# Kernel tuning notes

Measured on AMD Instinct MI355X. Metric: run time of the kernel, lower is better.

## Reference

```python
import jax, jax.numpy as jnp
import numpy as np

NUM_CLASSES = 97  # vocab size; SOS token id == NUM_CLASSES
D = 512   # in_planes (xDim)
S = 512   # sDim (GRU hidden)
A = 512   # attDim == emdDim
T = 25    # max_len_labels == encoder length L
B = 2048  # batch


def setup_inputs() -> dict:
    key = jax.random.key(0)
    ks = jax.random.split(key, 15)
    r = lambda k, shp: jax.random.normal(k, shp, jnp.float32) * 0.05
    return dict(
        x=jax.random.normal(ks[0], (B, T, D), jnp.float32),
        targets=jax.random.randint(ks[1], (2, B, T), 0, NUM_CLASSES),  # (fwd, reversed)
        Wx=r(ks[2], (2, D, A)), bx=r(ks[3], (2, A)),
        Ws=r(ks[4], (2, S, A)), bs=r(ks[5], (2, A)),
        wv=r(ks[6], (2, A)), wvb=r(ks[7], (2,)),
        emb=r(ks[8], (2, NUM_CLASSES + 1, A)),
        Wih=r(ks[9], (2, 3 * S, D + A)), bih=r(ks[10], (2, 3 * S)),
        Whh=r(ks[11], (2, 3 * S, S)), bhh=r(ks[12], (2, 3 * S)),
        Wfc=r(ks[13], (2, NUM_CLASSES, S)), bfc=r(ks[14], (2, NUM_CLASSES)),
    )


def _decode(x, targets, Wx, bx, Ws, bs, wv, wvb, emb, Wih, bih, Whh, bhh, Wfc, bfc):
    """One DecoderUnit unrolled over T steps (teacher forcing). x: [B,L,D]."""
    Bn = x.shape[0]
    # xEmbed is step-invariant -> hoist out of the recurrence
    xProj = jnp.einsum('bld,da->bla', x, Wx) + bx  # [B,L,A]
    y0 = jnp.full((Bn, 1), NUM_CLASSES, dtype=targets.dtype)  # SOS at step 0
    y_seq = jnp.concatenate([y0, targets[:, :-1]], axis=1)     # [B,T]

    def step(s, y_prev):
        # Bahdanau attention
        sProj = s @ Ws + bs                                  # [B,A]
        e = jnp.tanh(sProj[:, None, :] + xProj) @ wv + wvb   # [B,L]
        alpha = jax.nn.softmax(e, axis=1)
        ctx = jnp.einsum('bl,bld->bd', alpha, x)             # [B,D]
        # single-step GRU (PyTorch gate convention: r, z, n)
        gin = jnp.concatenate([emb[y_prev], ctx], axis=1)    # [B, A+D]
        gi = gin @ Wih.T + bih                               # [B,3S]
        gh = s @ Whh.T + bhh
        ir, iz, inn = jnp.split(gi, 3, axis=1)
        hr, hz, hn = jnp.split(gh, 3, axis=1)
        r = jax.nn.sigmoid(ir + hr)
        z = jax.nn.sigmoid(iz + hz)
        n = jnp.tanh(inn + r * hn)
        s_new = (1.0 - z) * n + z * s
        return s_new, s_new @ Wfc.T + bfc                    # logits [B,C]

    s0 = jnp.zeros((Bn, S), x.dtype)
    _, outs = jax.lax.scan(step, s0, jnp.swapaxes(y_seq, 0, 1))  # [T,B,C]
    return jnp.swapaxes(outs, 0, 1)  # [B,T,C]


def reference(x, targets, Wx, bx, Ws, bs, wv, wvb, emb, Wih, bih, Whh, bhh, Wfc, bfc):
    # vmap over the 2 decoders (forward / reverse); x shared
    f = jax.vmap(_decode, in_axes=(None, 0) + (0,) * 13)
    return f(x, targets, Wx, bx, Ws, bs, wv, wvb, emb, Wih, bih, Whh, bhh, Wfc, bfc)  # [2,B,T,C]
```

## Files before the change

### kernel.cpp

```cpp
#include <hip/hip_runtime.h>
#include <hip/hip_fp16.h>

#define B_ 2048
#define T_ 25
#define CL_ 97

typedef float f32x4 __attribute__((ext_vector_type(4)));
typedef _Float16 f16x8 __attribute__((ext_vector_type(8)));
typedef _Float16 f16x2 __attribute__((ext_vector_type(2)));

#define DI static __device__ __forceinline__

DI float fast_tanh(float x) { return 1.0f - 2.0f / (__expf(2.0f * x) + 1.0f); }
DI float fast_sigm(float x) { return 1.0f / (1.0f + __expf(-x)); }


__global__ void k_convx(const float* __restrict__ x, _Float16* __restrict__ xh, int n8) {
    int i = blockIdx.x * 256 + threadIdx.x;
    if (i >= n8) return;
    const f32x4 v0 = *(const f32x4*)(x + (long long)i * 8);
    const f32x4 v1 = *(const f32x4*)(x + (long long)i * 8 + 4);
    f16x8 o;
    o[0] = (_Float16)v0[0]; o[1] = (_Float16)v0[1]; o[2] = (_Float16)v0[2]; o[3] = (_Float16)v0[3];
    o[4] = (_Float16)v1[0]; o[5] = (_Float16)v1[1]; o[6] = (_Float16)v1[2]; o[7] = (_Float16)v1[3];
    *(f16x8*)(xh + (long long)i * 8) = o;
}

__global__ void k_pack_w1(const float* __restrict__ Ws, const float* __restrict__ Whh,
                          const float* __restrict__ Wfc, const float* __restrict__ bs,
                          const float* __restrict__ bhh, const float* __restrict__ bfc,
                          _Float16* __restrict__ w1, float* __restrict__ b1) {
    int idx = blockIdx.x * 256 + threadIdx.x;
    if (idx >= 2 * 2176 * 64) return;
    const int k8 = idx & 63;
    const int n  = (idx >> 6) % 2176;
    const int g  = (idx >> 6) / 2176;
    const int k0 = k8 * 8;
    f16x8 o;
    if (n < 512) {
        const float* p = Ws + (long long)g * 512 * 512 + (long long)k0 * 512 + n;
        #pragma unroll
        for (int i = 0; i < 8; ++i) o[i] = (_Float16)p[(long long)i * 512];
    } else if (n < 2048) {
        const float* p = Whh + (long long)g * 1536 * 512 + (long long)(n - 512) * 512 + k0;
        #pragma unroll
        for (int i = 0; i < 8; ++i) o[i] = (_Float16)p[i];
    } else if (n < 2048 + CL_) {
        const float* p = Wfc + (long long)g * CL_ * 512 + (long long)(n - 2048) * 512 + k0;
        #pragma unroll
        for (int i = 0; i < 8; ++i) o[i] = (_Float16)p[i];
    } else {
        #pragma unroll
        for (int i = 0; i < 8; ++i) o[i] = (_Float16)0.0f;
    }
    *(f16x8*)(w1 + ((long long)g * 2176 + n) * 512 + k0) = o;
    if (k8 == 0) {
        float bv = (n < 512) ? bs[g * 512 + n]
                 : (n < 2048) ? bhh[g * 1536 + (n - 512)]
                 : (n < 2048 + CL_) ? bfc[g * CL_ + (n - 2048)] : 0.0f;
        b1[g * 2176 + n] = bv;
    }
}

__global__ void k_pack_w2(const float* __restrict__ Wih, _Float16* __restrict__ w2) {
    int idx = blockIdx.x * 256 + threadIdx.x;
    if (idx >= 2 * 1536 * 64) return;
    const int k8 = idx & 63;
    const int n  = (idx >> 6) % 1536;
    const int g  = (idx >> 6) / 1536;
    const int k0 = k8 * 8;
    const float* p = Wih + (long long)g * 1536 * 1024 + (long long)n * 1024 + 512 + k0;
    f16x8 o;
    #pragma unroll
    for (int i = 0; i < 8; ++i) o[i] = (_Float16)p[i];
    *(f16x8*)(w2 + ((long long)g * 1536 + n) * 512 + k0) = o;
}

__global__ void k_pack_wx(const float* __restrict__ Wx, _Float16* __restrict__ wx) {
    int idx = blockIdx.x * 256 + threadIdx.x;
    if (idx >= 2 * 512 * 64) return;
    const int k8 = idx & 63;
    const int n  = (idx >> 6) & 511;
    const int g  = (idx >> 6) >> 9;
    const int k0 = k8 * 8;
    const float* p = Wx + (long long)g * 512 * 512 + (long long)k0 * 512 + n;
    f16x8 o;
    #pragma unroll
    for (int i = 0; i < 8; ++i) o[i] = (_Float16)p[(long long)i * 512];
    *(f16x8*)(wx + ((long long)g * 512 + n) * 512 + k0) = o;
}

__global__ __launch_bounds__(256) void k_emb(const float* __restrict__ emb,
                                             const float* __restrict__ Wih,
                                             const float* __restrict__ bih,
                                             float* __restrict__ eW) {
    const int y = blockIdx.x;
    const int g = blockIdx.y;
    __shared__ float er[512];
    const int tid = threadIdx.x;
    for (int i = tid; i < 512; i += 256) er[i] = emb[(long long)(g * 98 + y) * 512 + i];
    __syncthreads();
    for (int j = tid; j < 1536; j += 256) {
        const float* wr = Wih + (long long)g * 1536 * 1024 + (long long)j * 1024;
        float acc = bih[g * 1536 + j];
        #pragma unroll 8
        for (int a = 0; a < 512; ++a) acc += er[a] * wr[a];
        eW[(long long)(g * 98 + y) * 1536 + j] = acc;
    }
}

__global__ __launch_bounds__(256) void gemm_bt(
    const _Float16* __restrict__ A, long long aG,
    const _Float16* __restrict__ B, long long bG,
    float* __restrict__ Cf, _Float16* __restrict__ Ch,
    long long cG, int ldc,
    const float* __restrict__ bias, int biasG,
    int nblk_off, int n_split,
    float* __restrict__ lout, int lcols, int lldc)
{
    __shared__ _Float16 As[128][72];
    __shared__ _Float16 Bs[128][72];
    const int g  = blockIdx.z;
    const int m0 = blockIdx.y * 128;
    const int n0 = (blockIdx.x + nblk_off) * 128;
    const _Float16* Ag = A + (long long)g * aG + (long long)m0 * 512;
    const _Float16* Bg = B + (long long)g * bG + (long long)n0 * 512;
    const int tid  = threadIdx.x;
    const int lane = tid & 63, w = tid >> 6;
    const int wr = w >> 1, wc = w & 1;
    const int lr = lane & 15, kg = lane >> 4;
    const int arow = tid >> 3;
    const int acol = (tid & 7) * 8;

    f32x4 acc[4][4];
    #pragma unroll
    for (int m = 0; m < 4; ++m)
        #pragma unroll
        for (int n = 0; n < 4; ++n) acc[m][n] = (f32x4)0.0f;

    for (int kt = 0; kt < 8; ++kt) {
        const int k0 = kt * 64;
        f16x8 ra[4], rb[4];
        #pragma unroll
        for (int i = 0; i < 4; ++i) {
            ra[i] = *(const f16x8*)(Ag + (long long)(arow + i * 32) * 512 + k0 + acol);
            rb[i] = *(const f16x8*)(Bg + (long long)(arow + i * 32) * 512 + k0 + acol);
        }
        __syncthreads();
        #pragma unroll
        for (int i = 0; i < 4; ++i) {
            *(f16x8*)&As[arow + i * 32][acol] = ra[i];
            *(f16x8*)&Bs[arow + i * 32][acol] = rb[i];
        }
        __syncthreads();
        #pragma unroll
        for (int kk = 0; kk < 2; ++kk) {
            f16x8 af[4], bf[4];
            #pragma unroll
            for (int m = 0; m < 4; ++m) af[m] = *(const f16x8*)&As[wr * 64 + m * 16 + lr][kk * 32 + kg * 8];
            #pragma unroll
            for (int n = 0; n < 4; ++n) bf[n] = *(const f16x8*)&Bs[wc * 64 + n * 16 + lr][kk * 32 + kg * 8];
            #pragma unroll
            for (int m = 0; m < 4; ++m)
                #pragma unroll
                for (int n = 0; n < 4; ++n)
                    acc[m][n] = __builtin_amdgcn_mfma_f32_16x16x32_f16(af[m], bf[n], acc[m][n], 0, 0, 0);
        }
    }

    #pragma unroll
    for (int n = 0; n < 4; ++n) {
        const int col = n0 + wc * 64 + n * 16 + lr;
        const float bb = bias ? bias[g * biasG + col] : 0.0f;
        if (col < n_split) {
            #pragma unroll
            for (int m = 0; m < 4; ++m) {
                const int row = m0 + wr * 64 + m * 16 + kg * 4;
                #pragma unroll
                for (int i = 0; i < 4; ++i) {
                    const long long off = (long long)g * cG + (long long)(row + i) * ldc + col;
                    const float v = acc[m][n][i] + bb;
                    if (Ch) Ch[off] = (_Float16)v; else Cf[off] = v;
                }
            }
        } else if (lout != nullptr) {
            const int c = col - n_split;
            if (c < lcols) {
                #pragma unroll
                for (int m = 0; m < 4; ++m) {
                    const int row = m0 + wr * 64 + m * 16 + kg * 4;
                    #pragma unroll
                    for (int i = 0; i < 4; ++i)
                        lout[(long long)(g * B_ + row + i) * lldc + c] = acc[m][n][i] + bb;
                }
            }
        }
    }
}

__global__ __launch_bounds__(256) void k_att(
    const float* __restrict__ Y,
    const _Float16* __restrict__ xpj,
    const _Float16* __restrict__ xh,
    const float* __restrict__ wv,
    _Float16* __restrict__ ctxh)
{
    const int b = blockIdx.x, g = blockIdx.z;
    const int tid = threadIdx.x, lane = tid & 63, w = tid >> 6;
    __shared__ float eL[25];
    const float* sp  = Y + (long long)(g * B_ + b) * 2048;
    const float* wvg = wv + g * 512;
    const int a0 = lane * 8;
    const f32x4 sp0 = *(const f32x4*)(sp + a0);
    const f32x4 sp1 = *(const f32x4*)(sp + a0 + 4);
    const f32x4 wv0 = *(const f32x4*)(wvg + a0);
    const f32x4 wv1 = *(const f32x4*)(wvg + a0 + 4);
    const _Float16* xpb = xpj + (long long)(g * B_ + b) * 25 * 512;
    for (int l = w; l < 25; l += 4) {
        const f16x8 xv = *(const f16x8*)(xpb + l * 512 + a0);
        float part = 0.0f;
        #pragma unroll
        for (int i = 0; i < 4; ++i) {
            part += fast_tanh(sp0[i] + (float)xv[i])     * wv0[i];
            part += fast_tanh(sp1[i] + (float)xv[4 + i]) * wv1[i];
        }
        #pragma unroll
        for (int off = 32; off > 0; off >>= 1) part += __shfl_xor(part, off);
        if (lane == 0) eL[l] = part;
    }
    __syncthreads();
    float m = -1e30f;
    #pragma unroll
    for (int l = 0; l < 25; ++l) m = fmaxf(m, eL[l]);
    float al[25], ssum = 0.0f;
    #pragma unroll
    for (int l = 0; l < 25; ++l) { al[l] = __expf(eL[l] - m); ssum += al[l]; }
    const float inv = 1.0f / ssum;
    const _Float16* xb = xh + (long long)b * 25 * 512;
    const int d0 = tid * 2;
    float c0 = 0.0f, c1 = 0.0f;
    #pragma unroll
    for (int l = 0; l < 25; ++l) {
        const f16x2 xv = *(const f16x2*)(xb + l * 512 + d0);
        c0 += al[l] * (float)xv[0];
        c1 += al[l] * (float)xv[1];
    }
    f16x2 o; o[0] = (_Float16)(c0 * inv); o[1] = (_Float16)(c1 * inv);
    *(f16x2*)(ctxh + (long long)(g * B_ + b) * 512 + d0) = o;
}

__global__ void k_gate(const float* __restrict__ Y,
                       const float* __restrict__ Y2,
                       const float* __restrict__ eW,
                       const int* __restrict__ tgt,
                       float* __restrict__ s32, _Float16* __restrict__ sh, int t)
{
    const int idx = blockIdx.x * 256 + threadIdx.x;
    if (idx >= 2 * B_ * 512) return;
    const int j = idx & 511;
    const int b = (idx >> 9) & (B_ - 1);
    const int g = idx >> 20;
    const int y = (t == 0) ? CL_ : tgt[(g * B_ + b) * T_ + t - 1];
    const float* ew = eW + (long long)(g * 98 + y) * 1536;
    const float* y2 = Y2 + (long long)(g * B_ + b) * 1536;
    const float* yy = Y  + (long long)(g * B_ + b) * 2048;
    const float r  = fast_sigm(ew[j]        + y2[j]        + yy[512 + j]);
    const float z  = fast_sigm(ew[512 + j]  + y2[512 + j]  + yy[1024 + j]);
    const float nn = fast_tanh(ew[1024 + j] + y2[1024 + j] + r * yy[1536 + j]);
    const long long si = (long long)(g * B_ + b) * 512 + j;
    const float sn = (1.0f - z) * nn + z * s32[si];
    s32[si] = sn;
    sh[si]  = (_Float16)sn;
}

extern "C" void kernel_launch(void* const* d_in, const int* in_sizes, int n_in,
                              void* d_out, int out_size, void* d_ws, size_t ws_size,
                              hipStream_t stream)
{
    (void)in_sizes; (void)n_in; (void)out_size;
    const float* x   = (const float*)d_in[0];
    const int*   tgt = (const int*)d_in[1];
    const float* Wx  = (const float*)d_in[2];
    const float* bx  = (const float*)d_in[3];
    const float* Wsm = (const float*)d_in[4];
    const float* bs  = (const float*)d_in[5];
    const float* wv  = (const float*)d_in[6];
    const float* emb = (const float*)d_in[8];
    const float* Wih = (const float*)d_in[9];
    const float* bih = (const float*)d_in[10];
    const float* Whh = (const float*)d_in[11];
    const float* bhh = (const float*)d_in[12];
    const float* Wfc = (const float*)d_in[13];
    const float* bfc = (const float*)d_in[14];
    float* out = (float*)d_out;

    char* base = (char*)d_ws;
    size_t off = 0;
    auto alloc = [&](size_t bytes) -> void* {
        void* r = base + off;
        off = (off + bytes + 255) & ~(size_t)255;
        return r;
    };
    _Float16* xh  = (_Float16*)alloc((size_t)B_ * T_ * 512 * 2);
    _Float16* xpj = (_Float16*)alloc((size_t)2 * B_ * T_ * 512 * 2);
    _Float16* w1  = (_Float16*)alloc((size_t)2 * 2176 * 512 * 2);
    _Float16* w2  = (_Float16*)alloc((size_t)2 * 1536 * 512 * 2);
    _Float16* wx  = (_Float16*)alloc((size_t)2 * 512 * 512 * 2);
    float*    b1  = (float*)alloc((size_t)2 * 2176 * 4);
    float*    eW  = (float*)alloc((size_t)2 * 98 * 1536 * 4);
    float*    s32 = (float*)alloc((size_t)2 * B_ * 512 * 4);
    _Float16* sh  = (_Float16*)alloc((size_t)2 * B_ * 512 * 2);
    _Float16* ctx = (_Float16*)alloc((size_t)2 * B_ * 512 * 2);
    float*    Y   = (float*)alloc((size_t)2 * B_ * 2048 * 4);
    float*    Y2  = (float*)alloc((size_t)2 * B_ * 1536 * 4);
    if (off > ws_size) return;

    hipMemsetAsync(s32, 0, (size_t)2 * B_ * 512 * 4, stream);
    hipMemsetAsync(sh,  0, (size_t)2 * B_ * 512 * 2, stream);

    k_convx  <<<12800, 256, 0, stream>>>(x, xh, (B_ * T_ * 512) / 8);
    k_pack_w1<<<1088, 256, 0, stream>>>(Wsm, Whh, Wfc, bs, bhh, bfc, w1, b1);
    k_pack_w2<<<768, 256, 0, stream>>>(Wih, w2);
    k_pack_wx<<<256, 256, 0, stream>>>(Wx, wx);
    k_emb    <<<dim3(98, 2), 256, 0, stream>>>(emb, Wih, bih, eW);

    gemm_bt<<<dim3(4, 400, 2), 256, 0, stream>>>(
        xh, 0ll, wx, 512ll * 512, nullptr, xpj, (long long)B_ * T_ * 512, 512,
        bx, 512, 0, 1 << 30, nullptr, 0, 0);

    for (int t = 0; t < T_; ++t) {
        gemm_bt<<<dim3(t > 0 ? 17 : 16, 16, 2), 256, 0, stream>>>(
            sh, (long long)B_ * 512, w1, 2176ll * 512, Y, nullptr,
            (long long)B_ * 2048, 2048, b1, 2176, 0, 2048,
            t > 0 ? out + (long long)(t - 1) * CL_ : nullptr, CL_, T_ * CL_);
        k_att<<<dim3(B_, 1, 2), 256, 0, stream>>>(Y, xpj, xh, wv, ctx);
        gemm_bt<<<dim3(12, 16, 2), 256, 0, stream>>>(
            ctx, (long long)B_ * 512, w2, 1536ll * 512, Y2, nullptr,
            (long long)B_ * 1536, 1536, nullptr, 0, 0, 1 << 30, nullptr, 0, 0);
        k_gate<<<8192, 256, 0, stream>>>(Y, Y2, eW, tgt, s32, sh, t);
    }
    gemm_bt<<<dim3(1, 16, 2), 256, 0, stream>>>(
        sh, (long long)B_ * 512, w1, 2176ll * 512, Y, nullptr,
        (long long)B_ * 2048, 2048, b1, 2176, 16, 2048,
        out + 24ll * CL_, CL_, T_ * CL_);
}
```

Before: 2.859 ms.

## Use direct global-to-LDS loads in GEMM, fp16 intermediates, MFMA embedding projection

The GEMM now stages tiles with global_load_lds (direct global-to-shared copies) into unpadded shared tiles, where before data went through registers. The per-step intermediates Y and Y2 are stored as fp16 instead of fp32, which roughly halves their traffic in the attention and gate kernels. The gate kernel processes two elements per thread. The scalar embedding×Wih precompute is replaced by a packed fp16 MFMA GEMM. Risks include LDS bank conflicts from removing the padding and reduced precision in the gate pre-activations.

```diff
diff --git a/kernel.cpp b/kernel.cpp
--- a/kernel.cpp
+++ b/kernel.cpp
@@ -6,6 +6,7 @@
 #define CL_ 97
 
 typedef float f32x4 __attribute__((ext_vector_type(4)));
+typedef float f32x2 __attribute__((ext_vector_type(2)));
 typedef _Float16 f16x8 __attribute__((ext_vector_type(8)));
 typedef _Float16 f16x2 __attribute__((ext_vector_type(2)));
 
@@ -13,6 +14,11 @@
 
 DI float fast_tanh(float x) { return 1.0f - 2.0f / (__expf(2.0f * x) + 1.0f); }
 DI float fast_sigm(float x) { return 1.0f / (1.0f + __expf(-x)); }
+
+DI void gl16(const void* g, void* l) {
+    __builtin_amdgcn_global_load_lds((const __attribute__((address_space(1))) void*)g,
+                                     (__attribute__((address_space(3))) void*)l, 16, 0, 0);
+}
 
 
 __global__ void k_convx(const float* __restrict__ x, _Float16* __restrict__ xh, int n8) {
@@ -62,18 +68,20 @@
     }
 }
 
-__global__ void k_pack_w2(const float* __restrict__ Wih, _Float16* __restrict__ w2) {
+__global__ void k_pack_w2(const float* __restrict__ Wih, _Float16* __restrict__ w2,
+                          _Float16* __restrict__ w2e) {
     int idx = blockIdx.x * 256 + threadIdx.x;
     if (idx >= 2 * 1536 * 64) return;
     const int k8 = idx & 63;
     const int n  = (idx >> 6) % 1536;
     const int g  = (idx >> 6) / 1536;
     const int k0 = k8 * 8;
-    const float* p = Wih + (long long)g * 1536 * 1024 + (long long)n * 1024 + 512 + k0;
-    f16x8 o;
-    #pragma unroll
-    for (int i = 0; i < 8; ++i) o[i] = (_Float16)p[i];
-    *(f16x8*)(w2 + ((long long)g * 1536 + n) * 512 + k0) = o;
+    const float* p = Wih + (long long)g * 1536 * 1024 + (long long)n * 1024;
+    f16x8 o, oe;
+    #pragma unroll
+    for (int i = 0; i < 8; ++i) { o[i] = (_Float16)p[512 + k0 + i]; oe[i] = (_Float16)p[k0 + i]; }
+    *(f16x8*)(w2  + ((long long)g * 1536 + n) * 512 + k0) = o;
+    *(f16x8*)(w2e + ((long long)g * 1536 + n) * 512 + k0) = oe;
 }
 
 __global__ void k_pack_wx(const float* __restrict__ Wx, _Float16* __restrict__ wx) {
@@ -90,23 +98,22 @@
     *(f16x8*)(wx + ((long long)g * 512 + n) * 512 + k0) = o;
 }
 
-__global__ __launch_bounds__(256) void k_emb(const float* __restrict__ emb,
-                                             const float* __restrict__ Wih,
-                                             const float* __restrict__ bih,
-                                             float* __restrict__ eW) {
-    const int y = blockIdx.x;
-    const int g = blockIdx.y;
-    __shared__ float er[512];
-    const int tid = threadIdx.x;
-    for (int i = tid; i < 512; i += 256) er[i] = emb[(long long)(g * 98 + y) * 512 + i];
-    __syncthreads();
-    for (int j = tid; j < 1536; j += 256) {
-        const float* wr = Wih + (long long)g * 1536 * 1024 + (long long)j * 1024;
-        float acc = bih[g * 1536 + j];
-        #pragma unroll 8
-        for (int a = 0; a < 512; ++a) acc += er[a] * wr[a];
-        eW[(long long)(g * 98 + y) * 1536 + j] = acc;
-    }
+__global__ void k_pack_emb(const float* __restrict__ emb, _Float16* __restrict__ embh) {
+    int i = blockIdx.x * 256 + threadIdx.x;
+    if (i >= 2 * 128 * 64) return;
+    const int k8 = i & 63;
+    const int y  = (i >> 6) & 127;
+    const int g  = i >> 13;
+    f16x8 o;
+    if (y < 98) {
+        const float* p = emb + (long long)(g * 98 + y) * 512 + k8 * 8;
+        #pragma unroll
+        for (int j = 0; j < 8; ++j) o[j] = (_Float16)p[j];
+    } else {
+        #pragma unroll
+        for (int j = 0; j < 8; ++j) o[j] = (_Float16)0.0f;
+    }
+    *(f16x8*)(embh + (long long)(g * 128 + y) * 512 + k8 * 8) = o;
 }
 
 __global__ __launch_bounds__(256) void gemm_bt(
@@ -118,8 +125,8 @@
     int nblk_off, int n_split,
     float* __restrict__ lout, int lcols, int lldc)
 {
-    __shared__ _Float16 As[128][72];
-    __shared__ _Float16 Bs[128][72];
+    __shared__ _Float16 As[128 * 64];
+    __shared__ _Float16 Bs[128 * 64];
     const int g  = blockIdx.z;
     const int m0 = blockIdx.y * 128;
     const int n0 = (blockIdx.x + nblk_off) * 128;
@@ -129,8 +136,8 @@
     const int lane = tid & 63, w = tid >> 6;
     const int wr = w >> 1, wc = w & 1;
     const int lr = lane & 15, kg = lane >> 4;
-    const int arow = tid >> 3;
-    const int acol = (tid & 7) * 8;
+    const int srow = (lane >> 3);
+    const int scol = (lane & 7) * 8;
 
     f32x4 acc[4][4];
     #pragma unroll
@@ -140,26 +147,21 @@
 
     for (int kt = 0; kt < 8; ++kt) {
         const int k0 = kt * 64;
-        f16x8 ra[4], rb[4];
-        #pragma unroll
-        for (int i = 0; i < 4; ++i) {
-            ra[i] = *(const f16x8*)(Ag + (long long)(arow + i * 32) * 512 + k0 + acol);
-            rb[i] = *(const f16x8*)(Bg + (long long)(arow + i * 32) * 512 + k0 + acol);
-        }
         __syncthreads();
         #pragma unroll
-        for (int i = 0; i < 4; ++i) {
-            *(f16x8*)&As[arow + i * 32][acol] = ra[i];
-            *(f16x8*)&Bs[arow + i * 32][acol] = rb[i];
+        for (int cc = 0; cc < 4; ++cc) {
+            const int r = w * 32 + cc * 8;
+            gl16(Ag + (long long)(r + srow) * 512 + k0 + scol, &As[r * 64]);
+            gl16(Bg + (long long)(r + srow) * 512 + k0 + scol, &Bs[r * 64]);
         }
         __syncthreads();
         #pragma unroll
         for (int kk = 0; kk < 2; ++kk) {
             f16x8 af[4], bf[4];
             #pragma unroll
-            for (int m = 0; m < 4; ++m) af[m] = *(const f16x8*)&As[wr * 64 + m * 16 + lr][kk * 32 + kg * 8];
+            for (int m = 0; m < 4; ++m) af[m] = *(const f16x8*)&As[(wr * 64 + m * 16 + lr) * 64 + kk * 32 + kg * 8];
             #pragma unroll
-            for (int n = 0; n < 4; ++n) bf[n] = *(const f16x8*)&Bs[wc * 64 + n * 16 + lr][kk * 32 + kg * 8];
+            for (int n = 0; n < 4; ++n) bf[n] = *(const f16x8*)&Bs[(wc * 64 + n * 16 + lr) * 64 + kk * 32 + kg * 8];
             #pragma unroll
             for (int m = 0; m < 4; ++m)
                 #pragma unroll
@@ -199,7 +201,7 @@
 }
 
 __global__ __launch_bounds__(256) void k_att(
-    const float* __restrict__ Y,
+    const _Float16* __restrict__ Yh,
     const _Float16* __restrict__ xpj,
     const _Float16* __restrict__ xh,
     const float* __restrict__ wv,
@@ -208,11 +210,10 @@
     const int b = blockIdx.x, g = blockIdx.z;
     const int tid = threadIdx.x, lane = tid & 63, w = tid >> 6;
     __shared__ float eL[25];
-    const float* sp  = Y + (long long)(g * B_ + b) * 2048;
+    const _Float16* sp = Yh + (long long)(g * B_ + b) * 2048;
     const float* wvg = wv + g * 512;
     const int a0 = lane * 8;
-    const f32x4 sp0 = *(const f32x4*)(sp + a0);
-    const f32x4 sp1 = *(const f32x4*)(sp + a0 + 4);
+    const f16x8 spv = *(const f16x8*)(sp + a0);
     const f32x4 wv0 = *(const f32x4*)(wvg + a0);
     const f32x4 wv1 = *(const f32x4*)(wvg + a0 + 4);
     const _Float16* xpb = xpj + (long long)(g * B_ + b) * 25 * 512;
@@ -221,8 +222,8 @@
         float part = 0.0f;
         #pragma unroll
         for (int i = 0; i < 4; ++i) {
-            part += fast_tanh(sp0[i] + (float)xv[i])     * wv0[i];
-            part += fast_tanh(sp1[i] + (float)xv[4 + i]) * wv1[i];
+            part += fast_tanh((float)spv[i]     + (float)xv[i])     * wv0[i];
+            part += fast_tanh((float)spv[4 + i] + (float)xv[4 + i]) * wv1[i];
         }
         #pragma unroll
         for (int off = 32; off > 0; off >>= 1) part += __shfl_xor(part, off);
@@ -249,28 +250,44 @@
     *(f16x2*)(ctxh + (long long)(g * B_ + b) * 512 + d0) = o;
 }
 
-__global__ void k_gate(const float* __restrict__ Y,
-                       const float* __restrict__ Y2,
+__global__ void k_gate(const _Float16* __restrict__ Yh,
+                       const _Float16* __restrict__ Y2h,
                        const float* __restrict__ eW,
                        const int* __restrict__ tgt,
                        float* __restrict__ s32, _Float16* __restrict__ sh, int t)
 {
     const int idx = blockIdx.x * 256 + threadIdx.x;
-    if (idx >= 2 * B_ * 512) return;
-    const int j = idx & 511;
-    const int b = (idx >> 9) & (B_ - 1);
-    const int g = idx >> 20;
-    const int y = (t == 0) ? CL_ : tgt[(g * B_ + b) * T_ + t - 1];
-    const float* ew = eW + (long long)(g * 98 + y) * 1536;
-    const float* y2 = Y2 + (long long)(g * B_ + b) * 1536;
-    const float* yy = Y  + (long long)(g * B_ + b) * 2048;
-    const float r  = fast_sigm(ew[j]        + y2[j]        + yy[512 + j]);
-    const float z  = fast_sigm(ew[512 + j]  + y2[512 + j]  + yy[1024 + j]);
-    const float nn = fast_tanh(ew[1024 + j] + y2[1024 + j] + r * yy[1536 + j]);
-    const long long si = (long long)(g * B_ + b) * 512 + j;
-    const float sn = (1.0f - z) * nn + z * s32[si];
-    s32[si] = sn;
-    sh[si]  = (_Float16)sn;
+    if (idx >= 2 * B_ * 256) return;
+    const int jp = (idx & 255) * 2;
+    const int b  = (idx >> 8) & (B_ - 1);
+    const int g  = idx >> 19;
+    const int y  = (t == 0) ? CL_ : tgt[(g * B_ + b) * T_ + t - 1];
+    const float*    ew = eW  + (long long)(g * 128 + y) * 1536;
+    const _Float16* y2 = Y2h + (long long)(g * B_ + b) * 1536;
+    const _Float16* yy = Yh  + (long long)(g * B_ + b) * 2048;
+    const f32x2 ewr = *(const f32x2*)(ew + jp);
+    const f32x2 ewz = *(const f32x2*)(ew + 512 + jp);
+    const f32x2 ewn = *(const f32x2*)(ew + 1024 + jp);
+    const f16x2 y2r = *(const f16x2*)(y2 + jp);
+    const f16x2 y2z = *(const f16x2*)(y2 + 512 + jp);
+    const f16x2 y2n = *(const f16x2*)(y2 + 1024 + jp);
+    const f16x2 ghr = *(const f16x2*)(yy + 512 + jp);
+    const f16x2 ghz = *(const f16x2*)(yy + 1024 + jp);
+    const f16x2 ghn = *(const f16x2*)(yy + 1536 + jp);
+    const long long si = (long long)(g * B_ + b) * 512 + jp;
+    const f32x2 so = *(const f32x2*)(s32 + si);
+    f32x2 sn;
+    f16x2 snh;
+    #pragma unroll
+    for (int i = 0; i < 2; ++i) {
+        const float r  = fast_sigm(ewr[i] + (float)y2r[i] + (float)ghr[i]);
+        const float z  = fast_sigm(ewz[i] + (float)y2z[i] + (float)ghz[i]);
+        const float nn = fast_tanh(ewn[i] + (float)y2n[i] + r * (float)ghn[i]);
+        sn[i]  = (1.0f - z) * nn + z * so[i];
+        snh[i] = (_Float16)sn[i];
+    }
+    *(f32x2*)(s32 + si) = sn;
+    *(f16x2*)(sh + si) = snh;
 }
 
 extern "C" void kernel_launch(void* const* d_in, const int* in_sizes, int n_in,
@@ -301,28 +318,34 @@
         off = (off + bytes + 255) & ~(size_t)255;
         return r;
     };
-    _Float16* xh  = (_Float16*)alloc((size_t)B_ * T_ * 512 * 2);
-    _Float16* xpj = (_Float16*)alloc((size_t)2 * B_ * T_ * 512 * 2);
-    _Float16* w1  = (_Float16*)alloc((size_t)2 * 2176 * 512 * 2);
-    _Float16* w2  = (_Float16*)alloc((size_t)2 * 1536 * 512 * 2);
-    _Float16* wx  = (_Float16*)alloc((size_t)2 * 512 * 512 * 2);
-    float*    b1  = (float*)alloc((size_t)2 * 2176 * 4);
-    float*    eW  = (float*)alloc((size_t)2 * 98 * 1536 * 4);
-    float*    s32 = (float*)alloc((size_t)2 * B_ * 512 * 4);
-    _Float16* sh  = (_Float16*)alloc((size_t)2 * B_ * 512 * 2);
-    _Float16* ctx = (_Float16*)alloc((size_t)2 * B_ * 512 * 2);
-    float*    Y   = (float*)alloc((size_t)2 * B_ * 2048 * 4);
-    float*    Y2  = (float*)alloc((size_t)2 * B_ * 1536 * 4);
+    _Float16* xh   = (_Float16*)alloc((size_t)B_ * T_ * 512 * 2);
+    _Float16* xpj  = (_Float16*)alloc((size_t)2 * B_ * T_ * 512 * 2);
+    _Float16* w1   = (_Float16*)alloc((size_t)2 * 2176 * 512 * 2);
+    _Float16* w2   = (_Float16*)alloc((size_t)2 * 1536 * 512 * 2);
+    _Float16* w2e  = (_Float16*)alloc((size_t)2 * 1536 * 512 * 2);
+    _Float16* wx   = (_Float16*)alloc((size_t)2 * 512 * 512 * 2);
+    _Float16* embh = (_Float16*)alloc((size_t)2 * 128 * 512 * 2);
+    float*    b1   = (float*)alloc((size_t)2 * 2176 * 4);
+    float*    eW   = (float*)alloc((size_t)2 * 128 * 1536 * 4);
+    float*    s32  = (float*)alloc((size_t)2 * B_ * 512 * 4);
+    _Float16* sh   = (_Float16*)alloc((size_t)2 * B_ * 512 * 2);
+    _Float16* ctx  = (_Float16*)alloc((size_t)2 * B_ * 512 * 2);
+    _Float16* Yh   = (_Float16*)alloc((size_t)2 * B_ * 2048 * 2);
+    _Float16* Y2h  = (_Float16*)alloc((size_t)2 * B_ * 1536 * 2);
     if (off > ws_size) return;
 
     hipMemsetAsync(s32, 0, (size_t)2 * B_ * 512 * 4, stream);
     hipMemsetAsync(sh,  0, (size_t)2 * B_ * 512 * 2, stream);
 
-    k_convx  <<<12800, 256, 0, stream>>>(x, xh, (B_ * T_ * 512) / 8);
-    k_pack_w1<<<1088, 256, 0, stream>>>(Wsm, Whh, Wfc, bs, bhh, bfc, w1, b1);
-    k_pack_w2<<<768, 256, 0, stream>>>(Wih, w2);
-    k_pack_wx<<<256, 256, 0, stream>>>(Wx, wx);
-    k_emb    <<<dim3(98, 2), 256, 0, stream>>>(emb, Wih, bih, eW);
+    k_convx   <<<12800, 256, 0, stream>>>(x, xh, (B_ * T_ * 512) / 8);
+    k_pack_w1 <<<1088, 256, 0, stream>>>(Wsm, Whh, Wfc, bs, bhh, bfc, w1, b1);
+    k_pack_w2 <<<768, 256, 0, stream>>>(Wih, w2, w2e);
+    k_pack_wx <<<256, 256, 0, stream>>>(Wx, wx);
+    k_pack_emb<<<64, 256, 0, stream>>>(emb, embh);
+
+    gemm_bt<<<dim3(12, 1, 2), 256, 0, stream>>>(
+        embh, 128ll * 512, w2e, 1536ll * 512, eW, nullptr,
+        128ll * 1536, 1536, bih, 1536, 0, 1 << 30, nullptr, 0, 0);
 
     gemm_bt<<<dim3(4, 400, 2), 256, 0, stream>>>(
         xh, 0ll, wx, 512ll * 512, nullptr, xpj, (long long)B_ * T_ * 512, 512,
@@ -330,17 +353,17 @@
 
     for (int t = 0; t < T_; ++t) {
         gemm_bt<<<dim3(t > 0 ? 17 : 16, 16, 2), 256, 0, stream>>>(
-            sh, (long long)B_ * 512, w1, 2176ll * 512, Y, nullptr,
+            sh, (long long)B_ * 512, w1, 2176ll * 512, nullptr, Yh,
             (long long)B_ * 2048, 2048, b1, 2176, 0, 2048,
             t > 0 ? out + (long long)(t - 1) * CL_ : nullptr, CL_, T_ * CL_);
-        k_att<<<dim3(B_, 1, 2), 256, 0, stream>>>(Y, xpj, xh, wv, ctx);
+        k_att<<<dim3(B_, 1, 2), 256, 0, stream>>>(Yh, xpj, xh, wv, ctx);
         gemm_bt<<<dim3(12, 16, 2), 256, 0, stream>>>(
-            ctx, (long long)B_ * 512, w2, 1536ll * 512, Y2, nullptr,
+            ctx, (long long)B_ * 512, w2, 1536ll * 512, nullptr, Y2h,
             (long long)B_ * 1536, 1536, nullptr, 0, 0, 1 << 30, nullptr, 0, 0);
-        k_gate<<<8192, 256, 0, stream>>>(Y, Y2, eW, tgt, s32, sh, t);
+        k_gate<<<4096, 256, 0, stream>>>(Yh, Y2h, eW, tgt, s32, sh, t);
     }
     gemm_bt<<<dim3(1, 16, 2), 256, 0, stream>>>(
-        sh, (long long)B_ * 512, w1, 2176ll * 512, Y, nullptr,
+        sh, (long long)B_ * 512, w1, 2176ll * 512, nullptr, Yh,
         (long long)B_ * 2048, 2048, b1, 2176, 16, 2048,
         out + 24ll * CL_, CL_, T_ * CL_);
 }
```

New measurement: 2.834 ms. About the same (-0.9%).
